# Kernel tuning notes

Hardware: AMD Instinct MI355X
Metric: run time of the kernel (lower is better)

## Reference

```python
import jax, jax.numpy as jnp
import numpy as np

N_NODES = 50000
N_EDGES = 800000
VOCAB = 4096
EMB = 128
HID = 128


def glorot(key, shape):
    limit = float(np.sqrt(6.0 / (shape[0] + shape[1])))
    return jax.random.uniform(key, shape, jnp.float32, -limit, limit)


def setup_inputs() -> dict:
    key = jax.random.key(0)
    k = jax.random.split(key, 6)
    x = jax.random.randint(k[0], (N_NODES, 1), 0, VOCAB, dtype=jnp.int64)
    edge_index = jax.random.randint(k[1], (2, N_EDGES), 0, N_NODES, dtype=jnp.int64)
    # Embedding init: normal(0, dim^-0.5)
    emb = jax.random.normal(k[2], (VOCAB, EMB), jnp.float32) * (EMB ** -0.5)
    W1 = glorot(k[3], (EMB, 2 * HID))
    b1 = jnp.zeros((2 * HID,), jnp.float32)
    W2 = glorot(k[4], (2 * HID, HID))
    b2 = jnp.zeros((HID,), jnp.float32)
    return {"x": x, "edge_index": edge_index, "emb": emb,
            "W1": W1, "b1": b1, "W2": W2, "b2": b2}


def _gcn_conv(h, src, dst, norm, W, b):
    # PyG GCNConv: transform then degree-normalized aggregate over A + I.
    h = h @ W                                   # [N, F_out]
    msg = norm[:, None] * h[src]                # [(E+N), F_out] gather
    out = jax.ops.segment_sum(msg, dst, num_segments=N_NODES)  # scatter-add
    return out + b


def _edges_with_self_loops_and_norm(edge_index):
    loop = jnp.arange(N_NODES, dtype=edge_index.dtype)
    src = jnp.concatenate([edge_index[0], loop])
    dst = jnp.concatenate([edge_index[1], loop])
    deg = jax.ops.segment_sum(jnp.ones_like(dst, jnp.float32), dst,
                              num_segments=N_NODES)
    inv_sqrt = jnp.where(deg > 0, deg ** -0.5, 0.0)
    norm = inv_sqrt[src] * inv_sqrt[dst]        # [(E+N)]
    return src, dst, norm


def reference(x, edge_index, emb, W1, b1, W2, b2):
    src, dst, norm = _edges_with_self_loops_and_norm(edge_index)
    h = emb[x[:, 0]]                            # embedding lookup + squeeze(1)
    h = jax.nn.relu(_gcn_conv(h, src, dst, norm, W1, b1))
    h = _gcn_conv(h, src, dst, norm, W2, b2)
    return h
```

## Files before the change

kernel.cpp:

```cpp
#include <hip/hip_runtime.h>


constexpr int FEAT = 128;
constexpr int HID2 = 256;
constexpr int CAP  = 64;

typedef __attribute__((ext_vector_type(8))) __bf16 bf16x8;
typedef __attribute__((ext_vector_type(4))) float f32x4;
typedef __attribute__((ext_vector_type(8))) _Float16 f16x8;
typedef __attribute__((ext_vector_type(4))) _Float16 f16x4;
union FragU { uint4 u; bf16x8 b; };
union H16 { _Float16 f; unsigned short u; };

__device__ inline void split_bf16_rne(float v, unsigned short& h, unsigned short& l) {
  unsigned u = __float_as_uint(v);
  unsigned short hh = (unsigned short)((u + 0x7FFFu + ((u >> 16) & 1u)) >> 16);
  float r = v - __uint_as_float(((unsigned)hh) << 16);
  unsigned u2 = __float_as_uint(r);
  unsigned short ll = (unsigned short)((u2 + 0x7FFFu + ((u2 >> 16) & 1u)) >> 16);
  h = hh; l = ll;
}

__device__ inline void split_trunc1(float v, unsigned short& h, unsigned short& l) {
  unsigned u = __float_as_uint(v);
  h = (unsigned short)(u >> 16);
  float r = v - __uint_as_float(u & 0xFFFF0000u);
  l = (unsigned short)(__float_as_uint(r) >> 16);
}


__global__ __launch_bounds__(256) void k_init_prep(int* cnt, int N, int nblkN,
    const float* __restrict__ W1, const float* __restrict__ W2,
    unsigned short* __restrict__ w1s_hi, unsigned short* __restrict__ w1s_lo,
    unsigned short* __restrict__ w2s_hi, unsigned short* __restrict__ w2s_lo) {
  int b = blockIdx.x;
  if (b < nblkN) {
    int i = b * 256 + threadIdx.x;
    if (i < N) cnt[i] = 0;
    return;
  }
  int idx = (b - nblkN) * 256 + threadIdx.x;
  unsigned short h, l;
  if (idx < FEAT * HID2) {
    int k = idx >> 8, n = idx & 255;
    split_bf16_rne(W1[idx], h, l);
    int t = n >> 4, lr = n & 15, kc = k >> 5, quad = (k >> 3) & 3, j = k & 7;
    int us = (((t * 4 + kc) * 64 + quad * 16 + lr) << 3) + j;
    w1s_hi[us] = h;
    w1s_lo[us] = l;
  } else {
    int jj = idx - FEAT * HID2;
    int k = jj >> 7, n = jj & 127;
    split_bf16_rne(W2[jj], h, l);
    int t = n >> 4, lr = n & 15, kc = k >> 5, quad = (k >> 3) & 3, j = k & 7;
    int us = (((t * 8 + kc) * 64 + quad * 16 + lr) << 3) + j;
    w2s_hi[us] = h;
    w2s_lo[us] = l;
  }
}


__global__ __launch_bounds__(256) void k_bucket(const int* __restrict__ src,
    const int* __restrict__ dst, int* cnt, unsigned short* csr, int E, int chunkN) {
  int g = blockIdx.x & 7;
  int e = (blockIdx.x >> 3) * 256 + threadIdx.x;
  if (e >= E) return;
  int d = dst[e];
  int lo = g * chunkN;
  if (d >= lo && d < lo + chunkN) {
    int pos = atomicAdd(&cnt[d], 1);
    if (pos < CAP) csr[d * CAP + pos] = (unsigned short)src[e];
  }
}


__global__ __launch_bounds__(256, 4) void k_gather_l1(const int* __restrict__ x,
    const float* __restrict__ emb, const int* __restrict__ cnt,
    const unsigned short* __restrict__ csr,
    unsigned short* __restrict__ aggf_hi, unsigned short* __restrict__ aggf_lo,
    int N) {
  int node = blockIdx.x * 16 + (threadIdx.x >> 4);
  if (node >= N) return;
  int c4 = (threadIdx.x & 15) * 4;
  int degN = cnt[node];
  float wd = rsqrtf((float)(degN + 1));
  int deg = degN > CAP ? CAP : degN;

  const float* e0 = &emb[(long long)x[node] * FEAT + c4];
  float4 aA = *reinterpret_cast<const float4*>(e0);
  float4 aB = *reinterpret_cast<const float4*>(e0 + 64);
  aA.x *= wd; aA.y *= wd; aA.z *= wd; aA.w *= wd;
  aB.x *= wd; aB.y *= wd; aB.z *= wd; aB.w *= wd;

  const unsigned short* row = csr + node * CAP;
  int j = 0;
  for (; j + 7 < deg; j += 8) {
    uint4 c8 = *reinterpret_cast<const uint4*>(row + j);
    int s[8] = {(int)(c8.x & 0xFFFF), (int)(c8.x >> 16),
                (int)(c8.y & 0xFFFF), (int)(c8.y >> 16),
                (int)(c8.z & 0xFFFF), (int)(c8.z >> 16),
                (int)(c8.w & 0xFFFF), (int)(c8.w >> 16)};
    const float* p[8];
    #pragma unroll
    for (int q = 0; q < 8; ++q) p[q] = &emb[(long long)x[s[q]] * FEAT + c4];
    float ws[8];
    #pragma unroll
    for (int q = 0; q < 8; ++q) ws[q] = rsqrtf((float)(cnt[s[q]] + 1));
    float4 rA[8], rB[8];
    #pragma unroll
    for (int q = 0; q < 8; ++q) {
      rA[q] = *reinterpret_cast<const float4*>(p[q]);
      rB[q] = *reinterpret_cast<const float4*>(p[q] + 64);
    }
    #pragma unroll
    for (int q = 0; q < 8; ++q) {
      aA.x += ws[q] * rA[q].x; aA.y += ws[q] * rA[q].y;
      aA.z += ws[q] * rA[q].z; aA.w += ws[q] * rA[q].w;
      aB.x += ws[q] * rB[q].x; aB.y += ws[q] * rB[q].y;
      aB.z += ws[q] * rB[q].z; aB.w += ws[q] * rB[q].w;
    }
  }
  if (j + 3 < deg) {
    uint2 c4e = *reinterpret_cast<const uint2*>(row + j);
    int s[4] = {(int)(c4e.x & 0xFFFF), (int)(c4e.x >> 16),
                (int)(c4e.y & 0xFFFF), (int)(c4e.y >> 16)};
    const float* p[4];
    #pragma unroll
    for (int q = 0; q < 4; ++q) p[q] = &emb[(long long)x[s[q]] * FEAT + c4];
    float ws[4];
    #pragma unroll
    for (int q = 0; q < 4; ++q) ws[q] = rsqrtf((float)(cnt[s[q]] + 1));
    float4 rA[4], rB[4];
    #pragma unroll
    for (int q = 0; q < 4; ++q) {
      rA[q] = *reinterpret_cast<const float4*>(p[q]);
      rB[q] = *reinterpret_cast<const float4*>(p[q] + 64);
    }
    #pragma unroll
    for (int q = 0; q < 4; ++q) {
      aA.x += ws[q] * rA[q].x; aA.y += ws[q] * rA[q].y;
      aA.z += ws[q] * rA[q].z; aA.w += ws[q] * rA[q].w;
      aB.x += ws[q] * rB[q].x; aB.y += ws[q] * rB[q].y;
      aB.z += ws[q] * rB[q].z; aB.w += ws[q] * rB[q].w;
    }
    j += 4;
  }
  for (; j < deg; ++j) {
    int s = row[j];
    float w = rsqrtf((float)(cnt[s] + 1));
    const float* p = &emb[(long long)x[s] * FEAT + c4];
    float4 a = *reinterpret_cast<const float4*>(p);
    float4 b = *reinterpret_cast<const float4*>(p + 64);
    aA.x += w * a.x; aA.y += w * a.y; aA.z += w * a.z; aA.w += w * a.w;
    aB.x += w * b.x; aB.y += w * b.y; aB.z += w * b.z; aB.w += w * b.w;
  }

  aA.x *= wd; aA.y *= wd; aA.z *= wd; aA.w *= wd;
  aB.x *= wd; aB.y *= wd; aB.z *= wd; aB.w *= wd;
  ushort4 hA, lA, hB, lB;
  split_bf16_rne(aA.x, hA.x, lA.x);
  split_bf16_rne(aA.y, hA.y, lA.y);
  split_bf16_rne(aA.z, hA.z, lA.z);
  split_bf16_rne(aA.w, hA.w, lA.w);
  split_bf16_rne(aB.x, hB.x, lB.x);
  split_bf16_rne(aB.y, hB.y, lB.y);
  split_bf16_rne(aB.z, hB.z, lB.z);
  split_bf16_rne(aB.w, hB.w, lB.w);

  int T = node >> 4, lr = node & 15;
  int kc = c4 >> 5, quad = (c4 >> 3) & 3, sub = c4 & 7;
  long long usA = (((long long)(T * 4 + kc) * 64 + quad * 16 + lr) << 3) + sub;
  long long usB = (((long long)(T * 4 + kc + 2) * 64 + quad * 16 + lr) << 3) + sub;
  *reinterpret_cast<ushort4*>(aggf_hi + usA) = hA;
  *reinterpret_cast<ushort4*>(aggf_lo + usA) = lA;
  *reinterpret_cast<ushort4*>(aggf_hi + usB) = hB;
  *reinterpret_cast<ushort4*>(aggf_lo + usB) = lB;
}


__global__ __launch_bounds__(256) void k_gather_l2(
    const unsigned short* __restrict__ hs2h,
    const int* __restrict__ cnt, const unsigned short* __restrict__ csr,
    const float* __restrict__ bias, float* __restrict__ out, int N, int Np) {
  int g    = blockIdx.x & 7;
  int half = g >> 2, qtr = g & 3;
  int Nq   = (N + 3) >> 2;
  int local = (blockIdx.x >> 3) * 32 + (threadIdx.x >> 3);
  if (local >= Nq) return;
  int node = qtr * Nq + local;
  if (node >= N) return;
  int f8 = (threadIdx.x & 7) * 8;
  const unsigned short* sl = hs2h + (long long)half * Np * 64;

  f32x4 a0, a1;
  {
    f16x8 v = *reinterpret_cast<const f16x8*>(sl + (long long)node * 64 + f8);
    a0 = __builtin_convertvector(__builtin_shufflevector(v, v, 0, 1, 2, 3), f32x4);
    a1 = __builtin_convertvector(__builtin_shufflevector(v, v, 4, 5, 6, 7), f32x4);
  }

  const unsigned short* row = csr + node * CAP;
  int degN = cnt[node];
  int deg = degN > CAP ? CAP : degN;
  int j = 0;
  for (; j + 15 < deg; j += 16) {
    uint4 c0 = *reinterpret_cast<const uint4*>(row + j);
    uint4 c1 = *reinterpret_cast<const uint4*>(row + j + 8);
    int s[16] = {(int)(c0.x & 0xFFFF), (int)(c0.x >> 16),
                 (int)(c0.y & 0xFFFF), (int)(c0.y >> 16),
                 (int)(c0.z & 0xFFFF), (int)(c0.z >> 16),
                 (int)(c0.w & 0xFFFF), (int)(c0.w >> 16),
                 (int)(c1.x & 0xFFFF), (int)(c1.x >> 16),
                 (int)(c1.y & 0xFFFF), (int)(c1.y >> 16),
                 (int)(c1.z & 0xFFFF), (int)(c1.z >> 16),
                 (int)(c1.w & 0xFFFF), (int)(c1.w >> 16)};
    f16x8 r[16];
    #pragma unroll
    for (int q = 0; q < 16; ++q)
      r[q] = *reinterpret_cast<const f16x8*>(sl + (long long)s[q] * 64 + f8);
    #pragma unroll
    for (int q = 0; q < 16; ++q) {
      a0 += __builtin_convertvector(__builtin_shufflevector(r[q], r[q], 0, 1, 2, 3), f32x4);
      a1 += __builtin_convertvector(__builtin_shufflevector(r[q], r[q], 4, 5, 6, 7), f32x4);
    }
  }
  if (j + 7 < deg) {
    uint4 c8 = *reinterpret_cast<const uint4*>(row + j);
    int s[8] = {(int)(c8.x & 0xFFFF), (int)(c8.x >> 16),
                (int)(c8.y & 0xFFFF), (int)(c8.y >> 16),
                (int)(c8.z & 0xFFFF), (int)(c8.z >> 16),
                (int)(c8.w & 0xFFFF), (int)(c8.w >> 16)};
    f16x8 r[8];
    #pragma unroll
    for (int q = 0; q < 8; ++q)
      r[q] = *reinterpret_cast<const f16x8*>(sl + (long long)s[q] * 64 + f8);
    #pragma unroll
    for (int q = 0; q < 8; ++q) {
      a0 += __builtin_convertvector(__builtin_shufflevector(r[q], r[q], 0, 1, 2, 3), f32x4);
      a1 += __builtin_convertvector(__builtin_shufflevector(r[q], r[q], 4, 5, 6, 7), f32x4);
    }
    j += 8;
  }
  if (j + 3 < deg) {
    uint2 c4e = *reinterpret_cast<const uint2*>(row + j);
    int s[4] = {(int)(c4e.x & 0xFFFF), (int)(c4e.x >> 16),
                (int)(c4e.y & 0xFFFF), (int)(c4e.y >> 16)};
    f16x8 r[4];
    #pragma unroll
    for (int q = 0; q < 4; ++q)
      r[q] = *reinterpret_cast<const f16x8*>(sl + (long long)s[q] * 64 + f8);
    #pragma unroll
    for (int q = 0; q < 4; ++q) {
      a0 += __builtin_convertvector(__builtin_shufflevector(r[q], r[q], 0, 1, 2, 3), f32x4);
      a1 += __builtin_convertvector(__builtin_shufflevector(r[q], r[q], 4, 5, 6, 7), f32x4);
    }
    j += 4;
  }
  for (; j < deg; ++j) {
    f16x8 v = *reinterpret_cast<const f16x8*>(sl + (long long)row[j] * 64 + f8);
    a0 += __builtin_convertvector(__builtin_shufflevector(v, v, 0, 1, 2, 3), f32x4);
    a1 += __builtin_convertvector(__builtin_shufflevector(v, v, 4, 5, 6, 7), f32x4);
  }

  float w = rsqrtf((float)(degN + 1));
  int col = half * 64 + f8;
  f32x4 b0 = *reinterpret_cast<const f32x4*>(&bias[col]);
  f32x4 b1v = *reinterpret_cast<const f32x4*>(&bias[col + 4]);
  a0 = a0 * w + b0;
  a1 = a1 * w + b1v;
  *reinterpret_cast<f32x4*>(&out[(long long)node * FEAT + col]) = a0;
  *reinterpret_cast<f32x4*>(&out[(long long)node * FEAT + col + 4]) = a1;
}


__global__ __launch_bounds__(256, 2) void k_mlp(
    const uint4* __restrict__ aggf_hi, const uint4* __restrict__ aggf_lo,
    const uint4* __restrict__ w1s_hi, const uint4* __restrict__ w1s_lo,
    const uint4* __restrict__ w2s_hi, const uint4* __restrict__ w2s_lo,
    const float* __restrict__ b1, const int* __restrict__ cnt,
    unsigned short* __restrict__ hs2h, int N, int Np) {
  __shared__ __align__(16) unsigned short h1h[32 * 256];
  __shared__ __align__(16) unsigned short h1l[32 * 256];

  int tid  = threadIdx.x;
  int wave = tid >> 6, lane = tid & 63, quad = lane >> 4, lr = lane & 15;
  int bid  = blockIdx.x;
  int m0 = bid * 32;
  int Tb = bid * 2;
  int rot1 = bid & 3;
  int ti0  = bid & 1;
  int kh0  = (bid >> 1) & 1;

  FragU a1h[2][4], a1l[2][4];
  #pragma unroll
  for (int rt = 0; rt < 2; ++rt)
    #pragma unroll
    for (int kc = 0; kc < 4; ++kc) {
      a1h[rt][kc].u = aggf_hi[(long long)((Tb + rt) * 4 + kc) * 64 + lane];
      a1l[rt][kc].u = aggf_lo[(long long)((Tb + rt) * 4 + kc) * 64 + lane];
    }

  FragU bh[2][4], bl[2][4];
  auto loadB1 = [&](int t, int buf) {
    #pragma unroll
    for (int kc = 0; kc < 4; ++kc) {
      bh[buf][kc].u = w1s_hi[(t * 4 + kc) * 64 + lane];
      bl[buf][kc].u = w1s_lo[(t * 4 + kc) * 64 + lane];
    }
  };
  auto comp1 = [&](int t, int buf) {
    f32x4 hh[2], hl[2], lh[2];
    #pragma unroll
    for (int rt = 0; rt < 2; ++rt) {
      hh[rt] = f32x4{0.f, 0.f, 0.f, 0.f};
      hl[rt] = f32x4{0.f, 0.f, 0.f, 0.f};
      lh[rt] = f32x4{0.f, 0.f, 0.f, 0.f};
    }
    #pragma unroll
    for (int kc = 0; kc < 4; ++kc)
      #pragma unroll
      for (int rt = 0; rt < 2; ++rt) {
        hh[rt] = __builtin_amdgcn_mfma_f32_16x16x32_bf16(a1h[rt][kc].b, bh[buf][kc].b, hh[rt], 0, 0, 0);
        hl[rt] = __builtin_amdgcn_mfma_f32_16x16x32_bf16(a1h[rt][kc].b, bl[buf][kc].b, hl[rt], 0, 0, 0);
        lh[rt] = __builtin_amdgcn_mfma_f32_16x16x32_bf16(a1l[rt][kc].b, bh[buf][kc].b, lh[rt], 0, 0, 0);
      }
    float bias = b1[t * 16 + lr];
    int c = t * 2 + (lr >> 3), jj = lr & 7;
    #pragma unroll
    for (int rt = 0; rt < 2; ++rt)
      #pragma unroll
      for (int r = 0; r < 4; ++r) {
        float v = hh[rt][r] + hl[rt][r] + lh[rt][r] + bias;
        v = v > 0.f ? v : 0.f;
        int row = rt * 16 + quad * 4 + r;
        int us = ((row * 32 + (c ^ (row & 7))) << 3) + jj;
        unsigned short sh, sl;
        split_trunc1(v, sh, sl);
        h1h[us] = sh;
        h1l[us] = sl;
      }
  };

  int t0 = wave * 4;
  loadB1(t0 + rot1, 0);
  #pragma unroll
  for (int i = 0; i < 4; ++i) {
    if (i < 3) loadB1(t0 + ((i + 1 + rot1) & 3), (i + 1) & 1);
    comp1(t0 + ((i + rot1) & 3), i & 1);
  }

  float inv_r[2][4];
  #pragma unroll
  for (int rt = 0; rt < 2; ++rt)
    #pragma unroll
    for (int r = 0; r < 4; ++r) {
      int gg = m0 + rt * 16 + quad * 4 + r;
      inv_r[rt][r] = rsqrtf((float)(cnt[gg < N ? gg : N - 1] + 1));
    }

  FragU pb2h[4], pb2l[4];
  {
    int t2p = wave * 2 + ti0;
    #pragma unroll
    for (int kc = 0; kc < 4; ++kc) {
      pb2h[kc].u = w2s_hi[(t2p * 8 + kh0 * 4 + kc) * 64 + lane];
      pb2l[kc].u = w2s_lo[(t2p * 8 + kh0 * 4 + kc) * 64 + lane];
    }
  }

  __syncthreads();

  #pragma unroll
  for (int tii = 0; tii < 2; ++tii) {
    int ti = ti0 ^ tii;
    int t2 = wave * 2 + ti;
    f32x4 hh[2], hl[2], lh[2];
    #pragma unroll
    for (int rt = 0; rt < 2; ++rt) {
      hh[rt] = f32x4{0.f, 0.f, 0.f, 0.f};
      hl[rt] = f32x4{0.f, 0.f, 0.f, 0.f};
      lh[rt] = f32x4{0.f, 0.f, 0.f, 0.f};
    }
    #pragma unroll
    for (int khi = 0; khi < 2; ++khi) {
      int kh = kh0 ^ khi;
      FragU b2h[4], b2l[4];
      if (tii == 0 && khi == 0) {
        #pragma unroll
        for (int kc = 0; kc < 4; ++kc) { b2h[kc] = pb2h[kc]; b2l[kc] = pb2l[kc]; }
      } else {
        #pragma unroll
        for (int kc = 0; kc < 4; ++kc) {
          b2h[kc].u = w2s_hi[(t2 * 8 + kh * 4 + kc) * 64 + lane];
          b2l[kc].u = w2s_lo[(t2 * 8 + kh * 4 + kc) * 64 + lane];
        }
      }
      FragU a2h[2][4], a2l[2][4];
      #pragma unroll
      for (int rt = 0; rt < 2; ++rt) {
        int row = rt * 16 + lr;
        #pragma unroll
        for (int kc = 0; kc < 4; ++kc) {
          int pc = (kh * 16 + kc * 4 + quad) ^ (row & 7);
          a2h[rt][kc].u = *reinterpret_cast<const uint4*>(&h1h[(row * 32 + pc) << 3]);
          a2l[rt][kc].u = *reinterpret_cast<const uint4*>(&h1l[(row * 32 + pc) << 3]);
        }
      }
      #pragma unroll
      for (int kc = 0; kc < 4; ++kc)
        #pragma unroll
        for (int rt = 0; rt < 2; ++rt) {
          hh[rt] = __builtin_amdgcn_mfma_f32_16x16x32_bf16(a2h[rt][kc].b, b2h[kc].b, hh[rt], 0, 0, 0);
          hl[rt] = __builtin_amdgcn_mfma_f32_16x16x32_bf16(a2h[rt][kc].b, b2l[kc].b, hl[rt], 0, 0, 0);
          lh[rt] = __builtin_amdgcn_mfma_f32_16x16x32_bf16(a2l[rt][kc].b, b2h[kc].b, lh[rt], 0, 0, 0);
        }
    }
    unsigned short* sl2 = hs2h + (long long)(t2 >> 2) * Np * 64 + (t2 & 3) * 16;
    #pragma unroll
    for (int rt = 0; rt < 2; ++rt)
      #pragma unroll
      for (int r = 0; r < 4; ++r) {
        int gg = m0 + rt * 16 + quad * 4 + r;
        if (gg < N) {
          float v = (hh[rt][r] + hl[rt][r] + lh[rt][r]) * inv_r[rt][r];
          H16 cv;
          cv.f = (_Float16)v;
          sl2[(long long)gg * 64 + lr] = cv.u;
        }
      }
  }
}


extern "C" void kernel_launch(void* const* d_in, const int* in_sizes, int n_in,
                              void* d_out, int out_size, void* d_ws, size_t ws_size,
                              hipStream_t stream) {
  const int*   x   = (const int*)d_in[0];
  const int*   ei  = (const int*)d_in[1];
  const float* emb = (const float*)d_in[2];
  const float* W1  = (const float*)d_in[3];
  const float* b1  = (const float*)d_in[4];
  const float* W2  = (const float*)d_in[5];
  const float* b2  = (const float*)d_in[6];
  float* out = (float*)d_out;

  const int N  = in_sizes[0];
  const int E  = in_sizes[1] / 2;
  const int nblk_mlp = (N + 31) / 32;
  const int Np = nblk_mlp * 32;
  const int chunkN = (N + 7) / 8;
  const int* src = ei;
  const int* dst = ei + E;

  int* cnt = (int*)d_ws;
  unsigned short* csr = (unsigned short*)(cnt + N);
  unsigned short* aggf_hi = csr + (long long)N * CAP;
  unsigned short* aggf_lo = aggf_hi + (long long)Np * FEAT;
  unsigned short* hs2h = aggf_lo + (long long)Np * FEAT;
  unsigned short* w1s_hi = hs2h + (long long)Np * FEAT;
  unsigned short* w1s_lo = w1s_hi + FEAT * HID2;
  unsigned short* w2s_hi = w1s_lo + FEAT * HID2;
  unsigned short* w2s_lo = w2s_hi + FEAT * HID2;

  const int Nq = (N + 3) / 4;
  const int nblk_N  = (N + 255) / 256;
  const int nblk_E8 = ((E + 255) / 256) * 8;
  const int nblk_g1 = (N + 15) / 16;
  const int nblk_g2 = ((Nq + 31) / 32) * 8;

  k_init_prep<<<nblk_N + 256, 256, 0, stream>>>(cnt, N, nblk_N, W1, W2,
                                                w1s_hi, w1s_lo, w2s_hi, w2s_lo);
  k_bucket<<<nblk_E8, 256, 0, stream>>>(src, dst, cnt, csr, E, chunkN);

  k_gather_l1<<<nblk_g1, 256, 0, stream>>>(x, emb, cnt, csr,
                                           aggf_hi, aggf_lo, N);
  k_mlp<<<nblk_mlp, 256, 0, stream>>>((const uint4*)aggf_hi, (const uint4*)aggf_lo,
                                      (const uint4*)w1s_hi, (const uint4*)w1s_lo,
                                      (const uint4*)w2s_hi, (const uint4*)w2s_lo,
                                      b1, cnt, hs2h, N, Np);
  k_gather_l2<<<nblk_g2, 256, 0, stream>>>(hs2h, cnt, csr, b2, out, N, Np);
}
```

Measured before the change: 225.1 us.

## Fuse layer-1 gather into MLP kernel via shared-memory aggregate staging

Merges the layer-1 neighbor gather kernel into the MLP kernel. Each block gathers its 32 nodes' aggregated embeddings into LDS in the MFMA fragment layout, then runs both matmuls from there. This removes the global round-trip of the hi/lo bf16 aggregate buffers and one kernel launch. In exchange, the latency-bound gather now runs inside a heavier kernel with more LDS and register use, at a declared occupancy of 3 blocks per CU.

New measurement: 212.9 us. 1.06x faster.

```diff
diff --git a/kernel.cpp b/kernel.cpp
--- a/kernel.cpp
+++ b/kernel.cpp
@@ -8,7 +8,6 @@
 typedef __attribute__((ext_vector_type(8))) __bf16 bf16x8;
 typedef __attribute__((ext_vector_type(4))) float f32x4;
 typedef __attribute__((ext_vector_type(8))) _Float16 f16x8;
-typedef __attribute__((ext_vector_type(4))) _Float16 f16x4;
 union FragU { uint4 u; bf16x8 b; };
 union H16 { _Float16 f; unsigned short u; };
 
@@ -74,107 +73,275 @@
 }
 
 
-__global__ __launch_bounds__(256, 4) void k_gather_l1(const int* __restrict__ x,
-    const float* __restrict__ emb, const int* __restrict__ cnt,
-    const unsigned short* __restrict__ csr,
-    unsigned short* __restrict__ aggf_hi, unsigned short* __restrict__ aggf_lo,
-    int N) {
-  int node = blockIdx.x * 16 + (threadIdx.x >> 4);
-  if (node >= N) return;
-  int c4 = (threadIdx.x & 15) * 4;
-  int degN = cnt[node];
-  float wd = rsqrtf((float)(degN + 1));
-  int deg = degN > CAP ? CAP : degN;
-
-  const float* e0 = &emb[(long long)x[node] * FEAT + c4];
-  float4 aA = *reinterpret_cast<const float4*>(e0);
-  float4 aB = *reinterpret_cast<const float4*>(e0 + 64);
-  aA.x *= wd; aA.y *= wd; aA.z *= wd; aA.w *= wd;
-  aB.x *= wd; aB.y *= wd; aB.z *= wd; aB.w *= wd;
-
-  const unsigned short* row = csr + node * CAP;
-  int j = 0;
-  for (; j + 7 < deg; j += 8) {
-    uint4 c8 = *reinterpret_cast<const uint4*>(row + j);
-    int s[8] = {(int)(c8.x & 0xFFFF), (int)(c8.x >> 16),
-                (int)(c8.y & 0xFFFF), (int)(c8.y >> 16),
-                (int)(c8.z & 0xFFFF), (int)(c8.z >> 16),
-                (int)(c8.w & 0xFFFF), (int)(c8.w >> 16)};
-    const float* p[8];
-    #pragma unroll
-    for (int q = 0; q < 8; ++q) p[q] = &emb[(long long)x[s[q]] * FEAT + c4];
-    float ws[8];
-    #pragma unroll
-    for (int q = 0; q < 8; ++q) ws[q] = rsqrtf((float)(cnt[s[q]] + 1));
-    float4 rA[8], rB[8];
-    #pragma unroll
-    for (int q = 0; q < 8; ++q) {
-      rA[q] = *reinterpret_cast<const float4*>(p[q]);
-      rB[q] = *reinterpret_cast<const float4*>(p[q] + 64);
-    }
-    #pragma unroll
-    for (int q = 0; q < 8; ++q) {
-      aA.x += ws[q] * rA[q].x; aA.y += ws[q] * rA[q].y;
-      aA.z += ws[q] * rA[q].z; aA.w += ws[q] * rA[q].w;
-      aB.x += ws[q] * rB[q].x; aB.y += ws[q] * rB[q].y;
-      aB.z += ws[q] * rB[q].z; aB.w += ws[q] * rB[q].w;
-    }
-  }
-  if (j + 3 < deg) {
-    uint2 c4e = *reinterpret_cast<const uint2*>(row + j);
-    int s[4] = {(int)(c4e.x & 0xFFFF), (int)(c4e.x >> 16),
-                (int)(c4e.y & 0xFFFF), (int)(c4e.y >> 16)};
-    const float* p[4];
-    #pragma unroll
-    for (int q = 0; q < 4; ++q) p[q] = &emb[(long long)x[s[q]] * FEAT + c4];
-    float ws[4];
-    #pragma unroll
-    for (int q = 0; q < 4; ++q) ws[q] = rsqrtf((float)(cnt[s[q]] + 1));
-    float4 rA[4], rB[4];
-    #pragma unroll
-    for (int q = 0; q < 4; ++q) {
-      rA[q] = *reinterpret_cast<const float4*>(p[q]);
-      rB[q] = *reinterpret_cast<const float4*>(p[q] + 64);
-    }
-    #pragma unroll
-    for (int q = 0; q < 4; ++q) {
-      aA.x += ws[q] * rA[q].x; aA.y += ws[q] * rA[q].y;
-      aA.z += ws[q] * rA[q].z; aA.w += ws[q] * rA[q].w;
-      aB.x += ws[q] * rB[q].x; aB.y += ws[q] * rB[q].y;
-      aB.z += ws[q] * rB[q].z; aB.w += ws[q] * rB[q].w;
-    }
-    j += 4;
-  }
-  for (; j < deg; ++j) {
-    int s = row[j];
-    float w = rsqrtf((float)(cnt[s] + 1));
-    const float* p = &emb[(long long)x[s] * FEAT + c4];
-    float4 a = *reinterpret_cast<const float4*>(p);
-    float4 b = *reinterpret_cast<const float4*>(p + 64);
-    aA.x += w * a.x; aA.y += w * a.y; aA.z += w * a.z; aA.w += w * a.w;
-    aB.x += w * b.x; aB.y += w * b.y; aB.z += w * b.z; aB.w += w * b.w;
-  }
-
-  aA.x *= wd; aA.y *= wd; aA.z *= wd; aA.w *= wd;
-  aB.x *= wd; aB.y *= wd; aB.z *= wd; aB.w *= wd;
-  ushort4 hA, lA, hB, lB;
-  split_bf16_rne(aA.x, hA.x, lA.x);
-  split_bf16_rne(aA.y, hA.y, lA.y);
-  split_bf16_rne(aA.z, hA.z, lA.z);
-  split_bf16_rne(aA.w, hA.w, lA.w);
-  split_bf16_rne(aB.x, hB.x, lB.x);
-  split_bf16_rne(aB.y, hB.y, lB.y);
-  split_bf16_rne(aB.z, hB.z, lB.z);
-  split_bf16_rne(aB.w, hB.w, lB.w);
-
-  int T = node >> 4, lr = node & 15;
-  int kc = c4 >> 5, quad = (c4 >> 3) & 3, sub = c4 & 7;
-  long long usA = (((long long)(T * 4 + kc) * 64 + quad * 16 + lr) << 3) + sub;
-  long long usB = (((long long)(T * 4 + kc + 2) * 64 + quad * 16 + lr) << 3) + sub;
-  *reinterpret_cast<ushort4*>(aggf_hi + usA) = hA;
-  *reinterpret_cast<ushort4*>(aggf_lo + usA) = lA;
-  *reinterpret_cast<ushort4*>(aggf_hi + usB) = hB;
-  *reinterpret_cast<ushort4*>(aggf_lo + usB) = lB;
+__global__ __launch_bounds__(256, 3) void k_gmlp(
+    const int* __restrict__ x, const float* __restrict__ emb,
+    const int* __restrict__ cnt, const unsigned short* __restrict__ csr,
+    const uint4* __restrict__ w1s_hi, const uint4* __restrict__ w1s_lo,
+    const uint4* __restrict__ w2s_hi, const uint4* __restrict__ w2s_lo,
+    const float* __restrict__ b1,
+    unsigned short* __restrict__ hs2h, int N, int Np) {
+  __shared__ __align__(16) unsigned short aggh[2 * 4 * 64 * 8];
+  __shared__ __align__(16) unsigned short aggl[2 * 4 * 64 * 8];
+  __shared__ __align__(16) unsigned short h1h[32 * 256];
+  __shared__ __align__(16) unsigned short h1l[32 * 256];
+
+  int tid  = threadIdx.x;
+  int wave = tid >> 6, lane = tid & 63, quad = lane >> 4, lr = lane & 15;
+  int bid  = blockIdx.x;
+  int m0 = bid * 32;
+  int rot1 = bid & 3;
+  int ti0  = bid & 1;
+  int kh0  = (bid >> 1) & 1;
+
+  int glr = tid >> 4;
+  int c4  = (tid & 15) * 4;
+  int kcg = c4 >> 5, qdg = (c4 >> 3) & 3, sub = c4 & 7;
+
+  #pragma unroll
+  for (int g = 0; g < 2; ++g) {
+    int node = m0 + g * 16 + glr;
+    int usA = (((g * 4 + kcg) * 64 + qdg * 16 + glr) << 3) + sub;
+    int usB = (((g * 4 + kcg + 2) * 64 + qdg * 16 + glr) << 3) + sub;
+    if (node < N) {
+      int degN = cnt[node];
+      float wd = rsqrtf((float)(degN + 1));
+      int deg = degN > CAP ? CAP : degN;
+
+      const float* e0 = &emb[(long long)x[node] * FEAT + c4];
+      float4 aA = *reinterpret_cast<const float4*>(e0);
+      float4 aB = *reinterpret_cast<const float4*>(e0 + 64);
+      aA.x *= wd; aA.y *= wd; aA.z *= wd; aA.w *= wd;
+      aB.x *= wd; aB.y *= wd; aB.z *= wd; aB.w *= wd;
+
+      const unsigned short* row = csr + node * CAP;
+      int j = 0;
+      for (; j + 7 < deg; j += 8) {
+        uint4 c8 = *reinterpret_cast<const uint4*>(row + j);
+        int s[8] = {(int)(c8.x & 0xFFFF), (int)(c8.x >> 16),
+                    (int)(c8.y & 0xFFFF), (int)(c8.y >> 16),
+                    (int)(c8.z & 0xFFFF), (int)(c8.z >> 16),
+                    (int)(c8.w & 0xFFFF), (int)(c8.w >> 16)};
+        const float* p[8];
+        #pragma unroll
+        for (int q = 0; q < 8; ++q) p[q] = &emb[(long long)x[s[q]] * FEAT + c4];
+        float ws[8];
+        #pragma unroll
+        for (int q = 0; q < 8; ++q) ws[q] = rsqrtf((float)(cnt[s[q]] + 1));
+        float4 rA[8], rB[8];
+        #pragma unroll
+        for (int q = 0; q < 8; ++q) {
+          rA[q] = *reinterpret_cast<const float4*>(p[q]);
+          rB[q] = *reinterpret_cast<const float4*>(p[q] + 64);
+        }
+        #pragma unroll
+        for (int q = 0; q < 8; ++q) {
+          aA.x += ws[q] * rA[q].x; aA.y += ws[q] * rA[q].y;
+          aA.z += ws[q] * rA[q].z; aA.w += ws[q] * rA[q].w;
+          aB.x += ws[q] * rB[q].x; aB.y += ws[q] * rB[q].y;
+          aB.z += ws[q] * rB[q].z; aB.w += ws[q] * rB[q].w;
+        }
+      }
+      if (j + 3 < deg) {
+        uint2 c4e = *reinterpret_cast<const uint2*>(row + j);
+        int s[4] = {(int)(c4e.x & 0xFFFF), (int)(c4e.x >> 16),
+                    (int)(c4e.y & 0xFFFF), (int)(c4e.y >> 16)};
+        const float* p[4];
+        #pragma unroll
+        for (int q = 0; q < 4; ++q) p[q] = &emb[(long long)x[s[q]] * FEAT + c4];
+        float ws[4];
+        #pragma unroll
+        for (int q = 0; q < 4; ++q) ws[q] = rsqrtf((float)(cnt[s[q]] + 1));
+        float4 rA[4], rB[4];
+        #pragma unroll
+        for (int q = 0; q < 4; ++q) {
+          rA[q] = *reinterpret_cast<const float4*>(p[q]);
+          rB[q] = *reinterpret_cast<const float4*>(p[q] + 64);
+        }
+        #pragma unroll
+        for (int q = 0; q < 4; ++q) {
+          aA.x += ws[q] * rA[q].x; aA.y += ws[q] * rA[q].y;
+          aA.z += ws[q] * rA[q].z; aA.w += ws[q] * rA[q].w;
+          aB.x += ws[q] * rB[q].x; aB.y += ws[q] * rB[q].y;
+          aB.z += ws[q] * rB[q].z; aB.w += ws[q] * rB[q].w;
+        }
+        j += 4;
+      }
+      for (; j < deg; ++j) {
+        int s = row[j];
+        float w = rsqrtf((float)(cnt[s] + 1));
+        const float* p = &emb[(long long)x[s] * FEAT + c4];
+        float4 a = *reinterpret_cast<const float4*>(p);
+        float4 b = *reinterpret_cast<const float4*>(p + 64);
+        aA.x += w * a.x; aA.y += w * a.y; aA.z += w * a.z; aA.w += w * a.w;
+        aB.x += w * b.x; aB.y += w * b.y; aB.z += w * b.z; aB.w += w * b.w;
+      }
+
+      aA.x *= wd; aA.y *= wd; aA.z *= wd; aA.w *= wd;
+      aB.x *= wd; aB.y *= wd; aB.z *= wd; aB.w *= wd;
+      ushort4 hA, lA, hB, lB;
+      split_bf16_rne(aA.x, hA.x, lA.x);
+      split_bf16_rne(aA.y, hA.y, lA.y);
+      split_bf16_rne(aA.z, hA.z, lA.z);
+      split_bf16_rne(aA.w, hA.w, lA.w);
+      split_bf16_rne(aB.x, hB.x, lB.x);
+      split_bf16_rne(aB.y, hB.y, lB.y);
+      split_bf16_rne(aB.z, hB.z, lB.z);
+      split_bf16_rne(aB.w, hB.w, lB.w);
+      *reinterpret_cast<ushort4*>(aggh + usA) = hA;
+      *reinterpret_cast<ushort4*>(aggl + usA) = lA;
+      *reinterpret_cast<ushort4*>(aggh + usB) = hB;
+      *reinterpret_cast<ushort4*>(aggl + usB) = lB;
+    } else {
+      ushort4 z = {0, 0, 0, 0};
+      *reinterpret_cast<ushort4*>(aggh + usA) = z;
+      *reinterpret_cast<ushort4*>(aggl + usA) = z;
+      *reinterpret_cast<ushort4*>(aggh + usB) = z;
+      *reinterpret_cast<ushort4*>(aggl + usB) = z;
+    }
+  }
+
+  FragU bh[2][4], bl[2][4];
+  auto loadB1 = [&](int t, int buf) {
+    #pragma unroll
+    for (int kc = 0; kc < 4; ++kc) {
+      bh[buf][kc].u = w1s_hi[(t * 4 + kc) * 64 + lane];
+      bl[buf][kc].u = w1s_lo[(t * 4 + kc) * 64 + lane];
+    }
+  };
+  int t0 = wave * 4;
+  loadB1(t0 + rot1, 0);
+
+  __syncthreads();
+
+  FragU a1h[2][4], a1l[2][4];
+  #pragma unroll
+  for (int rt = 0; rt < 2; ++rt)
+    #pragma unroll
+    for (int kc = 0; kc < 4; ++kc) {
+      int us = ((rt * 4 + kc) * 64 + lane) << 3;
+      a1h[rt][kc].u = *reinterpret_cast<const uint4*>(aggh + us);
+      a1l[rt][kc].u = *reinterpret_cast<const uint4*>(aggl + us);
+    }
+
+  auto comp1 = [&](int t, int buf) {
+    f32x4 hh[2], hl[2], lh[2];
+    #pragma unroll
+    for (int rt = 0; rt < 2; ++rt) {
+      hh[rt] = f32x4{0.f, 0.f, 0.f, 0.f};
+      hl[rt] = f32x4{0.f, 0.f, 0.f, 0.f};
+      lh[rt] = f32x4{0.f, 0.f, 0.f, 0.f};
+    }
+    #pragma unroll
+    for (int kc = 0; kc < 4; ++kc)
+      #pragma unroll
+      for (int rt = 0; rt < 2; ++rt) {
+        hh[rt] = __builtin_amdgcn_mfma_f32_16x16x32_bf16(a1h[rt][kc].b, bh[buf][kc].b, hh[rt], 0, 0, 0);
+        hl[rt] = __builtin_amdgcn_mfma_f32_16x16x32_bf16(a1h[rt][kc].b, bl[buf][kc].b, hl[rt], 0, 0, 0);
+        lh[rt] = __builtin_amdgcn_mfma_f32_16x16x32_bf16(a1l[rt][kc].b, bh[buf][kc].b, lh[rt], 0, 0, 0);
+      }
+    float bias = b1[t * 16 + lr];
+    int c = t * 2 + (lr >> 3), jj = lr & 7;
+    #pragma unroll
+    for (int rt = 0; rt < 2; ++rt)
+      #pragma unroll
+      for (int r = 0; r < 4; ++r) {
+        float v = hh[rt][r] + hl[rt][r] + lh[rt][r] + bias;
+        v = v > 0.f ? v : 0.f;
+        int row = rt * 16 + quad * 4 + r;
+        int us = ((row * 32 + (c ^ (row & 7))) << 3) + jj;
+        unsigned short sh, sl;
+        split_trunc1(v, sh, sl);
+        h1h[us] = sh;
+        h1l[us] = sl;
+      }
+  };
+
+  #pragma unroll
+  for (int i = 0; i < 4; ++i) {
+    if (i < 3) loadB1(t0 + ((i + 1 + rot1) & 3), (i + 1) & 1);
+    comp1(t0 + ((i + rot1) & 3), i & 1);
+  }
+
+  float inv_r[2][4];
+  #pragma unroll
+  for (int rt = 0; rt < 2; ++rt)
+    #pragma unroll
+    for (int r = 0; r < 4; ++r) {
+      int gg = m0 + rt * 16 + quad * 4 + r;
+      inv_r[rt][r] = rsqrtf((float)(cnt[gg < N ? gg : N - 1] + 1));
+    }
+
+  FragU pb2h[4], pb2l[4];
+  {
+    int t2p = wave * 2 + ti0;
+    #pragma unroll
+    for (int kc = 0; kc < 4; ++kc) {
+      pb2h[kc].u = w2s_hi[(t2p * 8 + kh0 * 4 + kc) * 64 + lane];
+      pb2l[kc].u = w2s_lo[(t2p * 8 + kh0 * 4 + kc) * 64 + lane];
+    }
+  }
+
+  __syncthreads();
+
+  #pragma unroll
+  for (int tii = 0; tii < 2; ++tii) {
+    int ti = ti0 ^ tii;
+    int t2 = wave * 2 + ti;
+    f32x4 hh[2], hl[2], lh[2];
+    #pragma unroll
+    for (int rt = 0; rt < 2; ++rt) {
+      hh[rt] = f32x4{0.f, 0.f, 0.f, 0.f};
+      hl[rt] = f32x4{0.f, 0.f, 0.f, 0.f};
+      lh[rt] = f32x4{0.f, 0.f, 0.f, 0.f};
+    }
+    #pragma unroll
+    for (int khi = 0; khi < 2; ++khi) {
+      int kh = kh0 ^ khi;
+      FragU b2h[4], b2l[4];
+      if (tii == 0 && khi == 0) {
+        #pragma unroll
+        for (int kc = 0; kc < 4; ++kc) { b2h[kc] = pb2h[kc]; b2l[kc] = pb2l[kc]; }
+      } else {
+        #pragma unroll
+        for (int kc = 0; kc < 4; ++kc) {
+          b2h[kc].u = w2s_hi[(t2 * 8 + kh * 4 + kc) * 64 + lane];
+          b2l[kc].u = w2s_lo[(t2 * 8 + kh * 4 + kc) * 64 + lane];
+        }
+      }
+      FragU a2h[2][4], a2l[2][4];
+      #pragma unroll
+      for (int rt = 0; rt < 2; ++rt) {
+        int row = rt * 16 + lr;
+        #pragma unroll
+        for (int kc = 0; kc < 4; ++kc) {
+          int pc = (kh * 16 + kc * 4 + quad) ^ (row & 7);
+          a2h[rt][kc].u = *reinterpret_cast<const uint4*>(&h1h[(row * 32 + pc) << 3]);
+          a2l[rt][kc].u = *reinterpret_cast<const uint4*>(&h1l[(row * 32 + pc) << 3]);
+        }
+      }
+      #pragma unroll
+      for (int kc = 0; kc < 4; ++kc)
+        #pragma unroll
+        for (int rt = 0; rt < 2; ++rt) {
+          hh[rt] = __builtin_amdgcn_mfma_f32_16x16x32_bf16(a2h[rt][kc].b, b2h[kc].b, hh[rt], 0, 0, 0);
+          hl[rt] = __builtin_amdgcn_mfma_f32_16x16x32_bf16(a2h[rt][kc].b, b2l[kc].b, hl[rt], 0, 0, 0);
+          lh[rt] = __builtin_amdgcn_mfma_f32_16x16x32_bf16(a2l[rt][kc].b, b2h[kc].b, lh[rt], 0, 0, 0);
+        }
+    }
+    unsigned short* sl2 = hs2h + (long long)(t2 >> 2) * Np * 64 + (t2 & 3) * 16;
+    #pragma unroll
+    for (int rt = 0; rt < 2; ++rt)
+      #pragma unroll
+      for (int r = 0; r < 4; ++r) {
+        int gg = m0 + rt * 16 + quad * 4 + r;
+        if (gg < N) {
+          float v = (hh[rt][r] + hl[rt][r] + lh[rt][r]) * inv_r[rt][r];
+          H16 cv;
+          cv.f = (_Float16)v;
+          sl2[(long long)gg * 64 + lr] = cv.u;
+        }
+      }
+  }
 }
 
 
@@ -273,165 +440,6 @@
 }
 
 
-__global__ __launch_bounds__(256, 2) void k_mlp(
-    const uint4* __restrict__ aggf_hi, const uint4* __restrict__ aggf_lo,
-    const uint4* __restrict__ w1s_hi, const uint4* __restrict__ w1s_lo,
-    const uint4* __restrict__ w2s_hi, const uint4* __restrict__ w2s_lo,
-    const float* __restrict__ b1, const int* __restrict__ cnt,
-    unsigned short* __restrict__ hs2h, int N, int Np) {
-  __shared__ __align__(16) unsigned short h1h[32 * 256];
-  __shared__ __align__(16) unsigned short h1l[32 * 256];
-
-  int tid  = threadIdx.x;
-  int wave = tid >> 6, lane = tid & 63, quad = lane >> 4, lr = lane & 15;
-  int bid  = blockIdx.x;
-  int m0 = bid * 32;
-  int Tb = bid * 2;
-  int rot1 = bid & 3;
-  int ti0  = bid & 1;
-  int kh0  = (bid >> 1) & 1;
-
-  FragU a1h[2][4], a1l[2][4];
-  #pragma unroll
-  for (int rt = 0; rt < 2; ++rt)
-    #pragma unroll
-    for (int kc = 0; kc < 4; ++kc) {
-      a1h[rt][kc].u = aggf_hi[(long long)((Tb + rt) * 4 + kc) * 64 + lane];
-      a1l[rt][kc].u = aggf_lo[(long long)((Tb + rt) * 4 + kc) * 64 + lane];
-    }
-
-  FragU bh[2][4], bl[2][4];
-  auto loadB1 = [&](int t, int buf) {
-    #pragma unroll
-    for (int kc = 0; kc < 4; ++kc) {
-      bh[buf][kc].u = w1s_hi[(t * 4 + kc) * 64 + lane];
-      bl[buf][kc].u = w1s_lo[(t * 4 + kc) * 64 + lane];
-    }
-  };
-  auto comp1 = [&](int t, int buf) {
-    f32x4 hh[2], hl[2], lh[2];
-    #pragma unroll
-    for (int rt = 0; rt < 2; ++rt) {
-      hh[rt] = f32x4{0.f, 0.f, 0.f, 0.f};
-      hl[rt] = f32x4{0.f, 0.f, 0.f, 0.f};
-      lh[rt] = f32x4{0.f, 0.f, 0.f, 0.f};
-    }
-    #pragma unroll
-    for (int kc = 0; kc < 4; ++kc)
-      #pragma unroll
-      for (int rt = 0; rt < 2; ++rt) {
-        hh[rt] = __builtin_amdgcn_mfma_f32_16x16x32_bf16(a1h[rt][kc].b, bh[buf][kc].b, hh[rt], 0, 0, 0);
-        hl[rt] = __builtin_amdgcn_mfma_f32_16x16x32_bf16(a1h[rt][kc].b, bl[buf][kc].b, hl[rt], 0, 0, 0);
-        lh[rt] = __builtin_amdgcn_mfma_f32_16x16x32_bf16(a1l[rt][kc].b, bh[buf][kc].b, lh[rt], 0, 0, 0);
-      }
-    float bias = b1[t * 16 + lr];
-    int c = t * 2 + (lr >> 3), jj = lr & 7;
-    #pragma unroll
-    for (int rt = 0; rt < 2; ++rt)
-      #pragma unroll
-      for (int r = 0; r < 4; ++r) {
-        float v = hh[rt][r] + hl[rt][r] + lh[rt][r] + bias;
-        v = v > 0.f ? v : 0.f;
-        int row = rt * 16 + quad * 4 + r;
-        int us = ((row * 32 + (c ^ (row & 7))) << 3) + jj;
-        unsigned short sh, sl;
-        split_trunc1(v, sh, sl);
-        h1h[us] = sh;
-        h1l[us] = sl;
-      }
-  };
-
-  int t0 = wave * 4;
-  loadB1(t0 + rot1, 0);
-  #pragma unroll
-  for (int i = 0; i < 4; ++i) {
-    if (i < 3) loadB1(t0 + ((i + 1 + rot1) & 3), (i + 1) & 1);
-    comp1(t0 + ((i + rot1) & 3), i & 1);
-  }
-
-  float inv_r[2][4];
-  #pragma unroll
-  for (int rt = 0; rt < 2; ++rt)
-    #pragma unroll
-    for (int r = 0; r < 4; ++r) {
-      int gg = m0 + rt * 16 + quad * 4 + r;
-      inv_r[rt][r] = rsqrtf((float)(cnt[gg < N ? gg : N - 1] + 1));
-    }
-
-  FragU pb2h[4], pb2l[4];
-  {
-    int t2p = wave * 2 + ti0;
-    #pragma unroll
-    for (int kc = 0; kc < 4; ++kc) {
-      pb2h[kc].u = w2s_hi[(t2p * 8 + kh0 * 4 + kc) * 64 + lane];
-      pb2l[kc].u = w2s_lo[(t2p * 8 + kh0 * 4 + kc) * 64 + lane];
-    }
-  }
-
-  __syncthreads();
-
-  #pragma unroll
-  for (int tii = 0; tii < 2; ++tii) {
-    int ti = ti0 ^ tii;
-    int t2 = wave * 2 + ti;
-    f32x4 hh[2], hl[2], lh[2];
-    #pragma unroll
-    for (int rt = 0; rt < 2; ++rt) {
-      hh[rt] = f32x4{0.f, 0.f, 0.f, 0.f};
-      hl[rt] = f32x4{0.f, 0.f, 0.f, 0.f};
-      lh[rt] = f32x4{0.f, 0.f, 0.f, 0.f};
-    }
-    #pragma unroll
-    for (int khi = 0; khi < 2; ++khi) {
-      int kh = kh0 ^ khi;
-      FragU b2h[4], b2l[4];
-      if (tii == 0 && khi == 0) {
-        #pragma unroll
-        for (int kc = 0; kc < 4; ++kc) { b2h[kc] = pb2h[kc]; b2l[kc] = pb2l[kc]; }
-      } else {
-        #pragma unroll
-        for (int kc = 0; kc < 4; ++kc) {
-          b2h[kc].u = w2s_hi[(t2 * 8 + kh * 4 + kc) * 64 + lane];
-          b2l[kc].u = w2s_lo[(t2 * 8 + kh * 4 + kc) * 64 + lane];
-        }
-      }
-      FragU a2h[2][4], a2l[2][4];
-      #pragma unroll
-      for (int rt = 0; rt < 2; ++rt) {
-        int row = rt * 16 + lr;
-        #pragma unroll
-        for (int kc = 0; kc < 4; ++kc) {
-          int pc = (kh * 16 + kc * 4 + quad) ^ (row & 7);
-          a2h[rt][kc].u = *reinterpret_cast<const uint4*>(&h1h[(row * 32 + pc) << 3]);
-          a2l[rt][kc].u = *reinterpret_cast<const uint4*>(&h1l[(row * 32 + pc) << 3]);
-        }
-      }
-      #pragma unroll
-      for (int kc = 0; kc < 4; ++kc)
-        #pragma unroll
-        for (int rt = 0; rt < 2; ++rt) {
-          hh[rt] = __builtin_amdgcn_mfma_f32_16x16x32_bf16(a2h[rt][kc].b, b2h[kc].b, hh[rt], 0, 0, 0);
-          hl[rt] = __builtin_amdgcn_mfma_f32_16x16x32_bf16(a2h[rt][kc].b, b2l[kc].b, hl[rt], 0, 0, 0);
-          lh[rt] = __builtin_amdgcn_mfma_f32_16x16x32_bf16(a2l[rt][kc].b, b2h[kc].b, lh[rt], 0, 0, 0);
-        }
-    }
-    unsigned short* sl2 = hs2h + (long long)(t2 >> 2) * Np * 64 + (t2 & 3) * 16;
-    #pragma unroll
-    for (int rt = 0; rt < 2; ++rt)
-      #pragma unroll
-      for (int r = 0; r < 4; ++r) {
-        int gg = m0 + rt * 16 + quad * 4 + r;
-        if (gg < N) {
-          float v = (hh[rt][r] + hl[rt][r] + lh[rt][r]) * inv_r[rt][r];
-          H16 cv;
-          cv.f = (_Float16)v;
-          sl2[(long long)gg * 64 + lr] = cv.u;
-        }
-      }
-  }
-}
-
-
 extern "C" void kernel_launch(void* const* d_in, const int* in_sizes, int n_in,
                               void* d_out, int out_size, void* d_ws, size_t ws_size,
                               hipStream_t stream) {
@@ -454,9 +462,7 @@
 
   int* cnt = (int*)d_ws;
   unsigned short* csr = (unsigned short*)(cnt + N);
-  unsigned short* aggf_hi = csr + (long long)N * CAP;
-  unsigned short* aggf_lo = aggf_hi + (long long)Np * FEAT;
-  unsigned short* hs2h = aggf_lo + (long long)Np * FEAT;
+  unsigned short* hs2h = csr + (long long)N * CAP;
   unsigned short* w1s_hi = hs2h + (long long)Np * FEAT;
   unsigned short* w1s_lo = w1s_hi + FEAT * HID2;
   unsigned short* w2s_hi = w1s_lo + FEAT * HID2;
@@ -465,18 +471,15 @@
   const int Nq = (N + 3) / 4;
   const int nblk_N  = (N + 255) / 256;
   const int nblk_E8 = ((E + 255) / 256) * 8;
-  const int nblk_g1 = (N + 15) / 16;
   const int nblk_g2 = ((Nq + 31) / 32) * 8;
 
   k_init_prep<<<nblk_N + 256, 256, 0, stream>>>(cnt, N, nblk_N, W1, W2,
                                                 w1s_hi, w1s_lo, w2s_hi, w2s_lo);
   k_bucket<<<nblk_E8, 256, 0, stream>>>(src, dst, cnt, csr, E, chunkN);
 
-  k_gather_l1<<<nblk_g1, 256, 0, stream>>>(x, emb, cnt, csr,
-                                           aggf_hi, aggf_lo, N);
-  k_mlp<<<nblk_mlp, 256, 0, stream>>>((const uint4*)aggf_hi, (const uint4*)aggf_lo,
-                                      (const uint4*)w1s_hi, (const uint4*)w1s_lo,
-                                      (const uint4*)w2s_hi, (const uint4*)w2s_lo,
-                                      b1, cnt, hs2h, N, Np);
+  k_gmlp<<<nblk_mlp, 256, 0, stream>>>(x, emb, cnt, csr,
+                                       (const uint4*)w1s_hi, (const uint4*)w1s_lo,
+                                       (const uint4*)w2s_hi, (const uint4*)w2s_lo,
+                                       b1, hs2h, N, Np);
   k_gather_l2<<<nblk_g2, 256, 0, stream>>>(hs2h, cnt, csr, b2, out, N, Np);
 }
```
